# Performance work log

Measured on AMD Instinct MI355X. Metric: run time of the kernel, lower is better.

## Reference

```python
import jax, jax.numpy as jnp
import numpy as np

N_BINS = 64  # number of piecewise-linear bins; bins vector has N_BINS+1 boundaries
BATCH = 1_000_000


def setup_inputs() -> dict:
    key = jax.random.key(0)
    kx, kb = jax.random.split(key)
    x = jax.random.normal(kx, (BATCH, 1), dtype=jnp.float32)
    # sorted quantile-like boundaries (what adapt() would produce via np.quantile)
    bins = jnp.sort(jax.random.normal(kb, (N_BINS + 1,), dtype=jnp.float32))
    return {"x": x, "bins": bins}


def reference(x, bins):
    # x: [B, 1]; bins: [n_bins+1] sorted boundaries (lookup_table keys 0..n_bins)
    n_bins = bins.shape[0] - 1
    b_lo = bins[:-1]            # boundary[i-1] for bin i=1..n_bins -> [n_bins]
    b_hi = bins[1:]             # boundary[i]                      -> [n_bins]
    idx = jnp.arange(n_bins)    # i-1 in the original loop (i runs 1..n_bins)

    # left_mask_i  = (x < b[i-1]) & (i > 1)        -> idx > 0
    # right_mask_i = (x >= b[i])  & (i < n_bins)   -> idx < n_bins-1
    left = (x < b_lo) & (idx > 0)                  # [B, n_bins]
    right = (x >= b_hi) & (idx < n_bins - 1)       # [B, n_bins]
    v = (x - b_lo) / (b_hi - b_lo)                 # [B, n_bins]

    other = left == right                          # both False inside the bin
    enc = jnp.where(left, 0.0, 1.0)
    enc = jnp.where(other, v, enc)
    return enc.reshape(-1, 1, n_bins)              # [B, 1, n_bins]
```

## Files before the change

### kernel.cpp

```cpp
#include <hip/hip_runtime.h>

#define NB 64

typedef float vfloat4 __attribute__((ext_vector_type(4)));

__global__ __launch_bounds__(256) void ple_kernel(const float* __restrict__ x,
                                                  const float* __restrict__ bins,
                                                  float* __restrict__ out,
                                                  int batch) {
    __shared__ float s_lo[NB];
    __shared__ float s_hi[NB];

    const int tid = threadIdx.x;
    if (tid < NB) {
        s_lo[tid] = bins[tid];
        s_hi[tid] = bins[tid + 1];
    }
    __syncthreads();

    const long long t = (long long)blockIdx.x * blockDim.x + tid;
    const long long total4 = (long long)batch * (NB / 4);
    if (t >= total4) return;

    const int i  = (int)(t >> 4);
    const int j4 = ((int)t & 15) << 2;

    const float xv = x[i];

    const vfloat4 lo4 = *(const vfloat4*)&s_lo[j4];
    const vfloat4 hi4 = *(const vfloat4*)&s_hi[j4];

    vfloat4 r;
#pragma unroll
    for (int k = 0; k < 4; ++k) {
        const float lo = lo4[k];
        const float hi = hi4[k];
        const float v  = (xv - lo) / (hi - lo);
        const int j = j4 + k;
        r[k] = (xv < lo && j > 0) ? 0.0f : ((xv >= hi && j < NB - 1) ? 1.0f : v);
    }

    __builtin_nontemporal_store(r, (vfloat4*)out + t);
}

extern "C" void kernel_launch(void* const* d_in, const int* in_sizes, int n_in,
                              void* d_out, int out_size, void* d_ws, size_t ws_size,
                              hipStream_t stream) {
    const float* x    = (const float*)d_in[0];
    const float* bins = (const float*)d_in[1];
    float* out        = (float*)d_out;

    const int batch = in_sizes[0];
    const long long total4 = (long long)batch * (NB / 4);
    const int block = 256;
    const long long grid = (total4 + block - 1) / block;

    ple_kernel<<<(dim3)(unsigned)grid, block, 0, stream>>>(x, bins, out, batch);
}
```

Before: 287.0 us.

## Precompute reciprocal bin widths and clamp via min/max in a grid-stride loop

Each bin's reciprocal width and offset are computed once per block, so the per-element divide and compare/select chain becomes one FMA plus a min/max clamp, with sentinel clamp values standing in for the edge bins. The launch also switches to a fixed grid of 2048 blocks with a grid-stride loop, so the shared-memory setup is paid by fewer blocks. The clamp form and the reciprocal multiply can differ in rounding from the reference divide, and NaN or boundary-equality handling may not match exactly. The kernel writes 256 MB of output, so it is likely store-bound and the arithmetic savings may matter little.

After: 260.7 us. 9.2% less time.

```diff
diff --git a/kernel.cpp b/kernel.cpp
--- a/kernel.cpp
+++ b/kernel.cpp
@@ -1,4 +1,5 @@
 #include <hip/hip_runtime.h>
+#include <float.h>
 
 #define NB 64
 
@@ -7,40 +8,41 @@
 __global__ __launch_bounds__(256) void ple_kernel(const float* __restrict__ x,
                                                   const float* __restrict__ bins,
                                                   float* __restrict__ out,
-                                                  int batch) {
-    __shared__ float s_lo[NB];
-    __shared__ float s_hi[NB];
+                                                  long long total4) {
+    __shared__ __align__(16) float s_rinv[NB];
+    __shared__ __align__(16) float s_nlor[NB];
+    __shared__ __align__(16) float s_cl[NB];
+    __shared__ __align__(16) float s_ch[NB];
 
     const int tid = threadIdx.x;
     if (tid < NB) {
-        s_lo[tid] = bins[tid];
-        s_hi[tid] = bins[tid + 1];
+        const float lo   = bins[tid];
+        const float hi   = bins[tid + 1];
+        const float rinv = 1.0f / (hi - lo);
+        s_rinv[tid] = rinv;
+        s_nlor[tid] = -lo * rinv;
+        s_cl[tid] = (tid == 0)      ? -FLT_MAX : 0.0f;
+        s_ch[tid] = (tid == NB - 1) ?  FLT_MAX : 1.0f;
     }
     __syncthreads();
 
-    const long long t = (long long)blockIdx.x * blockDim.x + tid;
-    const long long total4 = (long long)batch * (NB / 4);
-    if (t >= total4) return;
+    const int j4 = (tid & 15) << 2;
+    const vfloat4 rinv4 = *(const vfloat4*)&s_rinv[j4];
+    const vfloat4 nlor4 = *(const vfloat4*)&s_nlor[j4];
+    const vfloat4 cl4   = *(const vfloat4*)&s_cl[j4];
+    const vfloat4 ch4   = *(const vfloat4*)&s_ch[j4];
 
-    const int i  = (int)(t >> 4);
-    const int j4 = ((int)t & 15) << 2;
-
-    const float xv = x[i];
-
-    const vfloat4 lo4 = *(const vfloat4*)&s_lo[j4];
-    const vfloat4 hi4 = *(const vfloat4*)&s_hi[j4];
-
-    vfloat4 r;
+    const long long stride = (long long)gridDim.x * blockDim.x;
+    for (long long t = (long long)blockIdx.x * blockDim.x + tid; t < total4; t += stride) {
+        const float xv = x[t >> 4];
+        vfloat4 r;
 #pragma unroll
-    for (int k = 0; k < 4; ++k) {
-        const float lo = lo4[k];
-        const float hi = hi4[k];
-        const float v  = (xv - lo) / (hi - lo);
-        const int j = j4 + k;
-        r[k] = (xv < lo && j > 0) ? 0.0f : ((xv >= hi && j < NB - 1) ? 1.0f : v);
+        for (int k = 0; k < 4; ++k) {
+            const float v = fmaf(xv, rinv4[k], nlor4[k]);
+            r[k] = fminf(fmaxf(v, cl4[k]), ch4[k]);
+        }
+        __builtin_nontemporal_store(r, (vfloat4*)out + t);
     }
-
-    __builtin_nontemporal_store(r, (vfloat4*)out + t);
 }
 
 extern "C" void kernel_launch(void* const* d_in, const int* in_sizes, int n_in,
@@ -52,8 +54,11 @@
 
     const int batch = in_sizes[0];
     const long long total4 = (long long)batch * (NB / 4);
+
     const int block = 256;
-    const long long grid = (total4 + block - 1) / block;
+    int grid = 2048;
+    const long long need = (total4 + block - 1) / block;
+    if (need < grid) grid = (int)need;
 
-    ple_kernel<<<(dim3)(unsigned)grid, block, 0, stream>>>(x, bins, out, batch);
+    ple_kernel<<<grid, block, 0, stream>>>(x, bins, out, total4);
 }
```
